# Performance work log

Hardware: AMD Instinct MI355X
Metric: run time of the kernel (lower is better)

Reference implementation:

```python
import jax, jax.numpy as jnp
import numpy as np

B, I, O, G, D = 2048, 128, 128, 8, 2  # batch, input_dim, output_dim, num_grids, num_dim (complex algebra)
RHO = 1.0
EPS = 1e-5  # BatchNorm1d default eps
GRID_MIN, GRID_MAX = -2.0, 2.0


def _make_cayley():
    # Complex-number geometric algebra: metric=[-1], basis {1, e1}, e1*e1 = -1.
    # (a*b)_z = sum_{x,y} a_x b_y C[x,y,z]
    C = np.zeros((2, 2, 2), dtype=np.float32)
    C[0, 0, 0] = 1.0
    C[0, 1, 1] = 1.0
    C[1, 0, 1] = 1.0
    C[1, 1, 0] = -1.0
    return jnp.asarray(C)


def _make_grid():
    # create_grid2d_full: real varies along axis 0, imag along axis 1 -> (G, G, 2)
    g = jnp.linspace(GRID_MIN, GRID_MAX, G)
    gr, gi = jnp.meshgrid(g, g, indexing='ij')
    return jnp.stack((gr, gi), axis=-1)


def setup_inputs() -> dict:
    key = jax.random.key(0)
    k1, k2 = jax.random.split(key)
    x = jax.random.normal(k1, (B, I, D), dtype=jnp.float32)
    weights = jax.random.normal(k2, (I, O, G, G, D), dtype=jnp.float32)
    silu_weight = jnp.ones((I, O, D), dtype=jnp.float32)
    silu_bias = jnp.zeros((I, O, D), dtype=jnp.float32)
    gamma = jnp.ones((D,), dtype=jnp.float32)   # BatchNorm weight (componentwise)
    beta = jnp.zeros((D,), dtype=jnp.float32)   # BatchNorm bias
    return {
        'x': x,
        'weights': weights,
        'silu_weight': silu_weight,
        'silu_bias': silu_bias,
        'gamma': gamma,
        'beta': beta,
        'grid': _make_grid(),
        'cayley': _make_cayley(),
    }


def reference(x, weights, silu_weight, silu_bias, gamma, beta, grid, cayley):
    # RBF expansion: exp(-||x - grid_point||^2 / rho), complex-algebra norm^2 = a^2 + b^2
    diff = x[:, :, None, None, :] - grid[None, None, :, :, :]        # (B, I, G, G, D)
    rbf = jnp.exp(-jnp.sum(diff * diff, axis=-1) / RHO)              # (B, I, G, G)
    # grid-weight contraction
    res = jnp.einsum('biuv,iouvx->biox', rbf, weights)               # (B, I, O, D)
    # componentwise SiLU branch with Cayley-table (complex) multiplication
    s = jax.nn.silu(x)                                               # (B, I, D)
    sv = jnp.einsum('iox,biy,xyz->bioz', silu_weight, s, cayley)     # (B, I, O, D)
    sv = sv + silu_bias
    out = jnp.sum(res + sv, axis=1)                                  # (B, O, D) -- 'biox->box'
    # componentwise BatchNorm (training mode): stats over (B, O) per component
    mean = jnp.mean(out, axis=(0, 1))
    var = jnp.var(out, axis=(0, 1))
    out = gamma * (out - mean) * jax.lax.rsqrt(var + EPS) + beta
    return out
```

## Files before the change

### kernel.cpp

```cpp
#include <hip/hip_runtime.h>
#include <stdint.h>

typedef unsigned short u16;
typedef __attribute__((ext_vector_type(8))) short bf16x8;
typedef __attribute__((ext_vector_type(4))) float f32x4;

#define B_      2048
#define I_      128
#define O_      128
#define K_MAIN  8192
#define K_TOT   8448
#define N_      256
#define BO      262144
#define NSLICE  8
#define KSTEPS  132

#define W_OFF      0u
#define W_BYTES    (256u*8448u*2u)
#define OUTPS_OFF  (W_OFF + W_BYTES)
#define OUTPS_BYTES (8u*524288u*4u)
#define OUTRED_OFF (OUTPS_OFF + OUTPS_BYTES)
#define OUTRED_BYTES (524288u*4u)
#define BSUM_OFF   (OUTRED_OFF + OUTRED_BYTES)
#define STATS_OFF  (BSUM_OFF + 1024u)

__device__ __forceinline__ float bf2f(u16 u) {
    union { unsigned int i; float f; } c; c.i = ((unsigned int)u) << 16; return c.f;
}
__device__ __forceinline__ u16 f2bf(float f) {
    unsigned int u = __float_as_uint(f);
    return (u16)((u + 0x7fffu + ((u >> 16) & 1u)) >> 16);
}
__device__ __forceinline__ float loadF(const void* p, long idx, bool isbf) {
    return isbf ? bf2f(((const u16*)p)[idx]) : ((const float*)p)[idx];
}

#define GLD16(gsrc, ldst) __builtin_amdgcn_global_load_lds( \
    (const __attribute__((address_space(1))) void*)(gsrc),  \
    (__attribute__((address_space(3))) void*)(ldst), 16, 0, 0)

__global__ __launch_bounds__(256) void pack_w(const void* wgt, const void* sw,
                                              const void* sb, u16* W, float* bsum,
                                              float* stats, const u16* flag) {
    bool isbf = (flag[0] == 0x3F80u);
    if (blockIdx.x < 1024) {
        int gid = blockIdx.x * 256 + threadIdx.x;
        int t8 = gid & 15;
        int io = gid >> 4;
        int i = io >> 7, o = io & 127;
        int base = t8 * 8;
        int u = base >> 4, v0 = (base & 15) >> 1;
        long off = ((long)i * 128 + o) * 128 + base;
        float f[8];
        if (isbf) {
            uint4 raw = *(const uint4*)((const u16*)wgt + off);
            const u16* h = (const u16*)&raw;
#pragma unroll
            for (int j = 0; j < 8; ++j) f[j] = bf2f(h[j]);
        } else {
            float4 a = *(const float4*)((const float*)wgt + off);
            float4 bq = *(const float4*)((const float*)wgt + off + 4);
            f[0]=a.x; f[1]=a.y; f[2]=a.z; f[3]=a.w;
            f[4]=bq.x; f[5]=bq.y; f[6]=bq.z; f[7]=bq.w;
        }
        u16 re[4], im[4];
#pragma unroll
        for (int j = 0; j < 4; ++j) { re[j] = f2bf(f[2*j]); im[j] = f2bf(f[2*j+1]); }
        int k = i * 64 + u * 8 + v0;
        *(uint2*)&W[(size_t)(2*o)     * K_TOT + k] = *(const uint2*)re;
        *(uint2*)&W[(size_t)(2*o + 1) * K_TOT + k] = *(const uint2*)im;
    } else if (blockIdx.x < 1280) {
        int e = (blockIdx.x - 1024) * 256 + threadIdx.x;
        int n = e >> 8, j = e & 255;
        int o = n >> 1, xc = n & 1;
        int i = j >> 1, c = j & 1;
        float swr = loadF(sw, (long)(i * 128 + o) * 2, isbf);
        float swi = loadF(sw, (long)(i * 128 + o) * 2 + 1, isbf);
        float v = (xc == 0) ? (c == 0 ? swr : -swi) : (c == 0 ? swi : swr);
        W[(size_t)n * K_TOT + K_MAIN + j] = f2bf(v);
    } else {
        int n = threadIdx.x;
        float s = 0.0f;
#pragma unroll 8
        for (int i = 0; i < 128; ++i) s += loadF(sb, (long)i * 256 + n, isbf);
        bsum[n] = s;
        if (threadIdx.x < 4) stats[threadIdx.x] = 0.0f;
    }
}

#define BM 128
#define BN 64
#define BK 64

__global__ __launch_bounds__(256, 2) void gemm_fused(const void* __restrict__ x,
                                                     const void* __restrict__ grd,
                                                     const u16* __restrict__ W,
                                                     float* __restrict__ out_ps,
                                                     const u16* flag) {
    bool isbf = (flag[0] == 0x3F80u);
    __shared__ u16 As[BM * BK];
    __shared__ u16 Bs[BN * BK];
    __shared__ float xs[128][17][2];
    int tid = threadIdx.x, lane = tid & 63, w = tid >> 6;
    int wm = w >> 1, wn = w & 1;
    int m0 = blockIdx.y * BM;
    int n0 = blockIdx.x * BN;
    int s = blockIdx.z;
    int quad = lane >> 4, l16 = lane & 15;
    int mrow = tid >> 1, h = tid & 1;
    int kbeg = (KSTEPS * s) / NSLICE, kend = (KSTEPS * (s + 1)) / NSLICE;
    int nrbf = (kend < 128 ? kend : 128) - kbeg;

    float g[8];
#pragma unroll
    for (int j = 0; j < 8; ++j) g[j] = loadF(grd, (long)j * 16, isbf);

    for (int t = h; t < nrbf; t += 2) {
        long base = ((long)(m0 + mrow) * 128 + kbeg + t) * 2;
        xs[mrow][t][0] = loadF(x, base, isbf);
        xs[mrow][t][1] = loadF(x, base + 1, isbf);
    }

    f32x4 zero = {0.f, 0.f, 0.f, 0.f};
    f32x4 acc[4][2];
#pragma unroll
    for (int mt = 0; mt < 4; ++mt)
#pragma unroll
        for (int nt = 0; nt < 2; ++nt) acc[mt][nt] = zero;

    __syncthreads();

    for (int kt = kbeg; kt < kend; ++kt) {
        int k0 = kt * 64;
#pragma unroll
        for (int jj = 0; jj < 2; ++jj) {
            int c = (w * 2 + jj) * 64 + lane;
            int row = c >> 3, col = c & 7;
            GLD16(W + (size_t)(n0 + row) * K_TOT + k0 + col * 8,
                  Bs + (size_t)(w * 2 + jj) * 512);
        }
        unsigned int op[16];
        if (kt < 128) {
            int t = kt - kbeg;
            float vr = xs[mrow][t][0], vi = xs[mrow][t][1];
            float ei[8];
#pragma unroll
            for (int v = 0; v < 8; ++v) { float d = vi - g[v]; ei[v] = __expf(-d * d); }
#pragma unroll
            for (int uu = 0; uu < 4; ++uu) {
                float d = vr - g[4 * h + uu];
                float er = __expf(-d * d);
#pragma unroll
                for (int v = 0; v < 8; v += 2) {
                    unsigned int lo = f2bf(er * ei[v]);
                    unsigned int hi = f2bf(er * ei[v + 1]);
                    op[uu * 4 + (v >> 1)] = lo | (hi << 16);
                }
            }
        } else {
            int t = kt - 128;
            long base = (long)(m0 + mrow) * 256 + 64 * t + 32 * h;
#pragma unroll
            for (int e = 0; e < 32; e += 2) {
                float v0 = loadF(x, base + e, isbf);
                float v1 = loadF(x, base + e + 1, isbf);
                float s0 = v0 / (1.0f + __expf(-v0));
                float s1 = v1 / (1.0f + __expf(-v1));
                op[e >> 1] = (unsigned int)f2bf(s0) | ((unsigned int)f2bf(s1) << 16);
            }
        }
        {
            u16* rowbase = As + mrow * 64;
            int sw7 = mrow & 7;
#pragma unroll
            for (int q = 0; q < 4; ++q)
                *(uint4*)(rowbase + (((4 * h + q) ^ sw7) << 3)) = ((const uint4*)op)[q];
        }
        __syncthreads();
#pragma unroll
        for (int ks = 0; ks < 2; ++ks) {
            bf16x8 fa[4], fb[2];
#pragma unroll
            for (int mt = 0; mt < 4; ++mt) {
                int r = wm * 64 + mt * 16 + l16;
                fa[mt] = *(const bf16x8*)&As[r * 64 + (((ks * 4 + quad) ^ (r & 7)) << 3)];
            }
#pragma unroll
            for (int nt = 0; nt < 2; ++nt)
                fb[nt] = *(const bf16x8*)&Bs[(wn * 32 + nt * 16 + l16) * BK + ks * 32 + quad * 8];
#pragma unroll
            for (int mt = 0; mt < 4; ++mt)
#pragma unroll
                for (int nt = 0; nt < 2; ++nt)
                    acc[mt][nt] = __builtin_amdgcn_mfma_f32_16x16x32_bf16(
                        fa[mt], fb[nt], acc[mt][nt], 0, 0, 0);
        }
        __syncthreads();
    }
    float* outp = out_ps + (size_t)s * 524288;
    int mbase = m0 + wm * 64 + quad * 4;
    int nbase = n0 + wn * 32 + l16;
#pragma unroll
    for (int mt = 0; mt < 4; ++mt)
#pragma unroll
        for (int nt = 0; nt < 2; ++nt) {
            int n = nbase + nt * 16;
#pragma unroll
            for (int r = 0; r < 4; ++r) {
                int m = mbase + mt * 16 + r;
                outp[(size_t)m * N_ + n] = acc[mt][nt][r];
            }
        }
}

__global__ void stats_red(const float* __restrict__ out_ps, const float* __restrict__ bsum,
                          float* __restrict__ out_red, float* stats) {
    int gid = blockIdx.x * 256 + threadIdx.x;
    int o = gid & 127;
    float vr = 0.f, vi = 0.f;
#pragma unroll
    for (int s = 0; s < NSLICE; ++s) {
        float2 p = *(const float2*)(out_ps + (size_t)s * 524288 + (size_t)gid * 2);
        vr += p.x; vi += p.y;
    }
    vr += bsum[o * 2]; vi += bsum[o * 2 + 1];
    float2 ov; ov.x = vr; ov.y = vi;
    *(float2*)(out_red + (size_t)gid * 2) = ov;
    float sr = vr, si = vi, qr = vr * vr, qi = vi * vi;
    for (int off = 32; off > 0; off >>= 1) {
        sr += __shfl_down(sr, off);
        si += __shfl_down(si, off);
        qr += __shfl_down(qr, off);
        qi += __shfl_down(qi, off);
    }
    __shared__ float red[4][4];
    int lane = threadIdx.x & 63, w = threadIdx.x >> 6;
    if (lane == 0) { red[w][0] = sr; red[w][1] = si; red[w][2] = qr; red[w][3] = qi; }
    __syncthreads();
    if (threadIdx.x < 4) {
        float t = red[0][threadIdx.x] + red[1][threadIdx.x] +
                  red[2][threadIdx.x] + red[3][threadIdx.x];
        atomicAdd(&stats[threadIdx.x], t);
    }
}

__global__ void norm_k(const float* __restrict__ out_red, const float* __restrict__ stats,
                       const void* gamma, const void* beta, void* out, const u16* flag) {
    bool isbf = (flag[0] == 0x3F80u);
    int gid = blockIdx.x * 256 + threadIdx.x;
    const float inv = 1.0f / (float)BO;
    float mr = stats[0] * inv, mi = stats[1] * inv;
    float varr = stats[2] * inv - mr * mr;
    float vari = stats[3] * inv - mi * mi;
    float gr = loadF(gamma, 0, isbf), gi = loadF(gamma, 1, isbf);
    float br = loadF(beta, 0, isbf),  bi = loadF(beta, 1, isbf);
    float scr = gr * rsqrtf(varr + 1e-5f);
    float sci = gi * rsqrtf(vari + 1e-5f);
    float2 v = *(const float2*)(out_red + (size_t)gid * 2);
    float rr = (v.x - mr) * scr + br;
    float ri = (v.y - mi) * sci + bi;
    if (isbf) {
        unsigned int packed = (unsigned int)f2bf(rr) | ((unsigned int)f2bf(ri) << 16);
        *(unsigned int*)((u16*)out + (size_t)gid * 2) = packed;
    } else {
        ((float*)out)[(size_t)gid * 2]     = rr;
        ((float*)out)[(size_t)gid * 2 + 1] = ri;
    }
}

extern "C" void kernel_launch(void* const* d_in, const int* in_sizes, int n_in,
                              void* d_out, int out_size, void* d_ws, size_t ws_size,
                              hipStream_t stream) {
    const void* x     = d_in[0];
    const void* wgt   = d_in[1];
    const void* sw    = d_in[2];
    const void* sb    = d_in[3];
    const void* gamma = d_in[4];
    const void* beta  = d_in[5];
    const void* grd   = d_in[6];
    const u16* flag = (const u16*)gamma;

    uint8_t* ws = (uint8_t*)d_ws;
    u16*   W       = (u16*)(ws + W_OFF);
    float* out_ps  = (float*)(ws + OUTPS_OFF);
    float* out_red = (float*)(ws + OUTRED_OFF);
    float* bsum    = (float*)(ws + BSUM_OFF);
    float* stats   = (float*)(ws + STATS_OFF);

    pack_w<<<1281, 256, 0, stream>>>(wgt, sw, sb, W, bsum, stats, flag);
    gemm_fused<<<dim3(N_ / BN, B_ / BM, NSLICE), 256, 0, stream>>>(x, grd, W, out_ps, flag);
    stats_red<<<1024, 256, 0, stream>>>(out_ps, bsum, out_red, stats);
    norm_k<<<1024, 256, 0, stream>>>(out_red, stats, gamma, beta, d_out, flag);
}
```

Measured before the change: 153.1 us.

## Reshape GEMM tile to 64x128, swizzle B tile, drop x staging in LDS

Changes the fused RBF-GEMM block tile from 128x64 to 64x128, so each block generates half as many RBF/SiLU A-rows and reuses them across twice as many output columns. The W tile loads into LDS are now XOR-swizzled to avoid bank conflicts on reads. The per-block x preload into shared memory is removed in favour of direct global loads each k-step. bf16 packing uses a perm instruction. The trade-off is more W traffic per block and reliance on launch grid dimensions matching the new tile sizes.

```diff
diff --git a/kernel.cpp b/kernel.cpp
--- a/kernel.cpp
+++ b/kernel.cpp
@@ -30,6 +30,12 @@
 __device__ __forceinline__ u16 f2bf(float f) {
     unsigned int u = __float_as_uint(f);
     return (u16)((u + 0x7fffu + ((u >> 16) & 1u)) >> 16);
+}
+__device__ __forceinline__ unsigned int pkbf(float lo, float hi) {
+    unsigned int ul = __float_as_uint(lo), uh = __float_as_uint(hi);
+    ul += 0x7fffu + ((ul >> 16) & 1u);
+    uh += 0x7fffu + ((uh >> 16) & 1u);
+    return __builtin_amdgcn_perm(uh, ul, 0x07060302);
 }
 __device__ __forceinline__ float loadF(const void* p, long idx, bool isbf) {
     return isbf ? bf2f(((const u16*)p)[idx]) : ((const float*)p)[idx];
@@ -88,8 +94,8 @@
     }
 }
 
-#define BM 128
-#define BN 64
+#define BM 64
+#define BN 128
 #define BK 64
 
 __global__ __launch_bounds__(256, 2) void gemm_fused(const void* __restrict__ x,
@@ -100,110 +106,100 @@
     bool isbf = (flag[0] == 0x3F80u);
     __shared__ u16 As[BM * BK];
     __shared__ u16 Bs[BN * BK];
-    __shared__ float xs[128][17][2];
     int tid = threadIdx.x, lane = tid & 63, w = tid >> 6;
     int wm = w >> 1, wn = w & 1;
     int m0 = blockIdx.y * BM;
     int n0 = blockIdx.x * BN;
     int s = blockIdx.z;
     int quad = lane >> 4, l16 = lane & 15;
-    int mrow = tid >> 1, h = tid & 1;
+    int arow = tid >> 2, q4 = tid & 3;
+    int asw = arow & 7;
     int kbeg = (KSTEPS * s) / NSLICE, kend = (KSTEPS * (s + 1)) / NSLICE;
-    int nrbf = (kend < 128 ? kend : 128) - kbeg;
 
     float g[8];
 #pragma unroll
     for (int j = 0; j < 8; ++j) g[j] = loadF(grd, (long)j * 16, isbf);
 
-    for (int t = h; t < nrbf; t += 2) {
-        long base = ((long)(m0 + mrow) * 128 + kbeg + t) * 2;
-        xs[mrow][t][0] = loadF(x, base, isbf);
-        xs[mrow][t][1] = loadF(x, base + 1, isbf);
-    }
-
     f32x4 zero = {0.f, 0.f, 0.f, 0.f};
-    f32x4 acc[4][2];
-#pragma unroll
-    for (int mt = 0; mt < 4; ++mt)
-#pragma unroll
-        for (int nt = 0; nt < 2; ++nt) acc[mt][nt] = zero;
-
-    __syncthreads();
+    f32x4 acc[2][4];
+#pragma unroll
+    for (int mt = 0; mt < 2; ++mt)
+#pragma unroll
+        for (int nt = 0; nt < 4; ++nt) acc[mt][nt] = zero;
 
     for (int kt = kbeg; kt < kend; ++kt) {
         int k0 = kt * 64;
 #pragma unroll
-        for (int jj = 0; jj < 2; ++jj) {
-            int c = (w * 2 + jj) * 64 + lane;
-            int row = c >> 3, col = c & 7;
-            GLD16(W + (size_t)(n0 + row) * K_TOT + k0 + col * 8,
-                  Bs + (size_t)(w * 2 + jj) * 512);
-        }
-        unsigned int op[16];
+        for (int jj = 0; jj < 4; ++jj) {
+            int p = (w * 4 + jj) * 64 + lane;
+            int r = p >> 3, cph = p & 7;
+            int c = cph ^ (r & 7);
+            GLD16(W + (size_t)(n0 + r) * K_TOT + k0 + c * 8,
+                  Bs + (size_t)p * 8);
+        }
+        unsigned int op[8];
         if (kt < 128) {
-            int t = kt - kbeg;
-            float vr = xs[mrow][t][0], vi = xs[mrow][t][1];
+            long xb = ((long)(m0 + arow) * 128 + kt) * 2;
+            float vr = loadF(x, xb, isbf);
+            float vi = loadF(x, xb + 1, isbf);
             float ei[8];
 #pragma unroll
             for (int v = 0; v < 8; ++v) { float d = vi - g[v]; ei[v] = __expf(-d * d); }
 #pragma unroll
-            for (int uu = 0; uu < 4; ++uu) {
-                float d = vr - g[4 * h + uu];
+            for (int uu = 0; uu < 2; ++uu) {
+                float d = vr - g[2 * q4 + uu];
                 float er = __expf(-d * d);
 #pragma unroll
-                for (int v = 0; v < 8; v += 2) {
-                    unsigned int lo = f2bf(er * ei[v]);
-                    unsigned int hi = f2bf(er * ei[v + 1]);
-                    op[uu * 4 + (v >> 1)] = lo | (hi << 16);
-                }
+                for (int v = 0; v < 8; v += 2)
+                    op[uu * 4 + (v >> 1)] = pkbf(er * ei[v], er * ei[v + 1]);
             }
         } else {
             int t = kt - 128;
-            long base = (long)(m0 + mrow) * 256 + 64 * t + 32 * h;
-#pragma unroll
-            for (int e = 0; e < 32; e += 2) {
+            long base = (long)(m0 + arow) * 256 + 64 * t + 16 * q4;
+#pragma unroll
+            for (int e = 0; e < 16; e += 2) {
                 float v0 = loadF(x, base + e, isbf);
                 float v1 = loadF(x, base + e + 1, isbf);
                 float s0 = v0 / (1.0f + __expf(-v0));
                 float s1 = v1 / (1.0f + __expf(-v1));
-                op[e >> 1] = (unsigned int)f2bf(s0) | ((unsigned int)f2bf(s1) << 16);
+                op[e >> 1] = pkbf(s0, s1);
             }
         }
         {
-            u16* rowbase = As + mrow * 64;
-            int sw7 = mrow & 7;
-#pragma unroll
-            for (int q = 0; q < 4; ++q)
-                *(uint4*)(rowbase + (((4 * h + q) ^ sw7) << 3)) = ((const uint4*)op)[q];
+            u16* rowbase = As + arow * 64;
+            *(uint4*)(rowbase + (((2 * q4)     ^ asw) << 3)) = ((const uint4*)op)[0];
+            *(uint4*)(rowbase + (((2 * q4 + 1) ^ asw) << 3)) = ((const uint4*)op)[1];
         }
         __syncthreads();
 #pragma unroll
         for (int ks = 0; ks < 2; ++ks) {
-            bf16x8 fa[4], fb[2];
-#pragma unroll
-            for (int mt = 0; mt < 4; ++mt) {
-                int r = wm * 64 + mt * 16 + l16;
+            bf16x8 fa[2], fb[4];
+#pragma unroll
+            for (int mt = 0; mt < 2; ++mt) {
+                int r = wm * 32 + mt * 16 + l16;
                 fa[mt] = *(const bf16x8*)&As[r * 64 + (((ks * 4 + quad) ^ (r & 7)) << 3)];
             }
 #pragma unroll
-            for (int nt = 0; nt < 2; ++nt)
-                fb[nt] = *(const bf16x8*)&Bs[(wn * 32 + nt * 16 + l16) * BK + ks * 32 + quad * 8];
-#pragma unroll
-            for (int mt = 0; mt < 4; ++mt)
-#pragma unroll
-                for (int nt = 0; nt < 2; ++nt)
+            for (int nt = 0; nt < 4; ++nt) {
+                int r = wn * 64 + nt * 16 + l16;
+                fb[nt] = *(const bf16x8*)&Bs[r * 64 + (((ks * 4 + quad) ^ (r & 7)) << 3)];
+            }
+#pragma unroll
+            for (int mt = 0; mt < 2; ++mt)
+#pragma unroll
+                for (int nt = 0; nt < 4; ++nt)
                     acc[mt][nt] = __builtin_amdgcn_mfma_f32_16x16x32_bf16(
                         fa[mt], fb[nt], acc[mt][nt], 0, 0, 0);
         }
         __syncthreads();
     }
     float* outp = out_ps + (size_t)s * 524288;
-    int mbase = m0 + wm * 64 + quad * 4;
-    int nbase = n0 + wn * 32 + l16;
-#pragma unroll
-    for (int mt = 0; mt < 4; ++mt)
-#pragma unroll
-        for (int nt = 0; nt < 2; ++nt) {
+    int mbase = m0 + wm * 32 + quad * 4;
+    int nbase = n0 + wn * 64 + l16;
+#pragma unroll
+    for (int mt = 0; mt < 2; ++mt)
+#pragma unroll
+        for (int nt = 0; nt < 4; ++nt) {
             int n = nbase + nt * 16;
 #pragma unroll
             for (int r = 0; r < 4; ++r) {
@@ -260,7 +256,7 @@
     float rr = (v.x - mr) * scr + br;
     float ri = (v.y - mi) * sci + bi;
     if (isbf) {
-        unsigned int packed = (unsigned int)f2bf(rr) | ((unsigned int)f2bf(ri) << 16);
+        unsigned int packed = pkbf(rr, ri);
         *(unsigned int*)((u16*)out + (size_t)gid * 2) = packed;
     } else {
         ((float*)out)[(size_t)gid * 2]     = rr;
```

Result: faster. 135.3 us (-11.7%).
